# Performance work log

Hardware: AMD Instinct MI355X
Metric: run time of the kernel (lower is better)

The kernel has to match this reference:

```python
import jax, jax.numpy as jnp
import numpy as np

B = 64        # number of graphs
NPG = 4096    # nodes per graph (equal-size segments, batch ids sorted)
H = 256       # hidden_dim
C0, C1 = 256, 64  # num_clusters


def setup_inputs() -> dict:
    key = jax.random.key(0)
    ks = jax.random.split(key, 8)
    N = B * NPG
    x = jax.random.normal(ks[0], (N, H), dtype=jnp.float32)
    edge_index = jax.random.randint(ks[1], (2, N), 0, N, dtype=jnp.int64)  # unused by forward
    batch = jnp.repeat(jnp.arange(B, dtype=jnp.int64), NPG)  # sorted, equal-size segments
    s = 1.0 / np.sqrt(H)
    W0 = jax.random.uniform(ks[2], (H, C0), jnp.float32, -s, s)
    b0 = jax.random.uniform(ks[3], (C0,), jnp.float32, -s, s)
    W1 = jax.random.uniform(ks[4], (H, C1), jnp.float32, -s, s)
    b1 = jax.random.uniform(ks[5], (C1,), jnp.float32, -s, s)
    sf = 1.0 / np.sqrt(C1 * H)
    Wf = jax.random.uniform(ks[6], (C1 * H, H), jnp.float32, -sf, sf)
    bf = jax.random.uniform(ks[7], (H,), jnp.float32, -sf, sf)
    return {"x": x, "edge_index": edge_index, "batch": batch,
            "W0": W0, "b0": b0, "W1": W1, "b1": b1, "Wf": Wf, "bf": bf}


def reference(x, edge_index, batch, W0, b0, W1, b1, Wf, bf):
    # Level 0: softmax cluster assignment + per-graph segmented matmul A^T @ F.
    # batch ids are sorted with equal-size segments, so the per-graph Python
    # loop of the original collapses to a reshape + batched einsum.
    A0 = jax.nn.softmax(x @ W0 + b0, axis=-1)                      # [N, C0]
    f0 = jnp.einsum('bnc,bnh->bch',
                    A0.reshape(B, NPG, C0),
                    x.reshape(B, NPG, H)).reshape(B * C0, H)        # [B*C0, H]
    # Level 1: same pattern on pooled cluster features (C0 'nodes' per graph).
    A1 = jax.nn.softmax(f0 @ W1 + b1, axis=-1)                     # [B*C0, C1]
    f1 = jnp.einsum('bnc,bnh->bch',
                    A1.reshape(B, C0, C1),
                    f0.reshape(B, C0, H)).reshape(B, C1 * H)        # [B, C1*H]
    # Final pool: Linear -> ReLU (Dropout is identity in eval mode).
    return jax.nn.relu(f1 @ Wf + bf)                               # [B, H]
```

## Files before the change

kernel.cpp:

```cpp
#include <hip/hip_runtime.h>
#include <stdint.h>

#define NG   64
#define NPG  4096
#define HD   256
#define NC0  256
#define NC1  64
#define KSPLIT 2

typedef __attribute__((ext_vector_type(8))) short bfx8;
typedef __attribute__((ext_vector_type(4))) float fx4;

__device__ __forceinline__ unsigned short f2bf(float f) {
  union { float f; unsigned int u; } v; v.f = f;
  return (unsigned short)((v.u + 0x7FFFu + ((v.u >> 16) & 1u)) >> 16);
}
__device__ __forceinline__ unsigned int pack2(float a, float b) {
  return (unsigned int)f2bf(a) | ((unsigned int)f2bf(b) << 16);
}

#define ASYNC_COPY16(gptr, lptr) \
  __builtin_amdgcn_global_load_lds((const __attribute__((address_space(1))) unsigned int*)(gptr), \
                                   (__attribute__((address_space(3))) unsigned int*)(lptr), 16, 0, 0)

__global__ __launch_bounds__(256) void k_w0f(const float* __restrict__ W0,
                                             unsigned short* __restrict__ W0F) {
  int gid = blockIdx.x * 256 + threadIdx.x;
  int l15 = gid & 15;
  int q   = (gid >> 4) & 3;
  int ks  = (gid >> 6) & 1;
  int kc  = (gid >> 7) & 3;
  int cblk = gid >> 9;
  int c = cblk * 16 + l15;
  int kb = kc * 64 + ks * 32 + q * 8;
  unsigned int u[4];
  #pragma unroll
  for (int j = 0; j < 8; j += 2)
    u[j >> 1] = pack2(W0[(size_t)(kb + j) * 256 + c], W0[(size_t)(kb + j + 1) * 256 + c]);
  *(float4*)(W0F + (size_t)gid * 8) = *(float4*)u;
}

#define XSP 72
__global__ __launch_bounds__(512, 2) void k_assign0(
    const float* __restrict__ x, const unsigned short* __restrict__ W0F,
    const float* __restrict__ b0, unsigned short* __restrict__ A0T,
    unsigned short* __restrict__ xT, int g0) {
  __shared__ unsigned short xs[2][128 * XSP];
  __shared__ float red[128 * 4];
  unsigned short* at = (unsigned short*)xs;

  int gl = blockIdx.x >> 5, nt = blockIdx.x & 31;
  int tid = threadIdx.x;
  int wave = tid >> 6, lane = tid & 63;
  int wm = wave >> 2, wn = wave & 3;
  int l15 = lane & 15, q = lane >> 4;

  fx4 acc[4][4];
  #pragma unroll
  for (int i = 0; i < 4; ++i)
    #pragma unroll
    for (int j = 0; j < 4; ++j) acc[i][j] = fx4{0.f, 0.f, 0.f, 0.f};

  const float* xbase = x + ((size_t)(g0 + gl) * NPG + (size_t)nt * 128) * HD;
  int snode = tid >> 2, sseg = (tid & 3) * 16;

  {
    const float4* src = (const float4*)(xbase + (size_t)snode * HD + sseg);
    float4 v0 = src[0], v1 = src[1], v2 = src[2], v3 = src[3];
    float4 pv[2]; unsigned int* pu = (unsigned int*)pv;
    pu[0] = pack2(v0.x, v0.y); pu[1] = pack2(v0.z, v0.w);
    pu[2] = pack2(v1.x, v1.y); pu[3] = pack2(v1.z, v1.w);
    pu[4] = pack2(v2.x, v2.y); pu[5] = pack2(v2.z, v2.w);
    pu[6] = pack2(v3.x, v3.y); pu[7] = pack2(v3.z, v3.w);
    float4* d = (float4*)&xs[0][snode * XSP + sseg];
    d[0] = pv[0]; d[1] = pv[1];
  }
  __syncthreads();

  for (int kc = 0; kc < 4; ++kc) {
    int buf = kc & 1;
    if (kc < 3) {
      const float4* src = (const float4*)(xbase + (size_t)snode * HD + (kc + 1) * 64 + sseg);
      float4 v0 = src[0], v1 = src[1], v2 = src[2], v3 = src[3];
      float4 pv[2]; unsigned int* pu = (unsigned int*)pv;
      pu[0] = pack2(v0.x, v0.y); pu[1] = pack2(v0.z, v0.w);
      pu[2] = pack2(v1.x, v1.y); pu[3] = pack2(v1.z, v1.w);
      pu[4] = pack2(v2.x, v2.y); pu[5] = pack2(v2.z, v2.w);
      pu[6] = pack2(v3.x, v3.y); pu[7] = pack2(v3.z, v3.w);
      float4* d = (float4*)&xs[buf ^ 1][snode * XSP + sseg];
      d[0] = pv[0]; d[1] = pv[1];
    }
    #pragma unroll
    for (int ks = 0; ks < 2; ++ks) {
      int kk = ks * 32 + q * 8;
      bfx8 af[4];
      #pragma unroll
      for (int mi = 0; mi < 4; ++mi)
        af[mi] = *(const bfx8*)&xs[buf][(wm * 64 + mi * 16 + l15) * XSP + kk];
      #pragma unroll
      for (int ni = 0; ni < 4; ++ni) {
        bfx8 bv = *(const bfx8*)(W0F + ((size_t)(((wn * 4 + ni) * 8 + kc * 2 + ks) * 64 + lane)) * 8);
        #pragma unroll
        for (int mi = 0; mi < 4; ++mi)
          acc[mi][ni] = __builtin_amdgcn_mfma_f32_16x16x32_bf16(af[mi], bv, acc[mi][ni], 0, 0, 0);
      }
    }
    {
      int hl = tid >> 3;
      int seg = (tid & 7) * 16;
      unsigned int u[8];
      #pragma unroll
      for (int i = 0; i < 16; i += 2) {
        unsigned short a = xs[buf][(seg + i) * XSP + hl];
        unsigned short b = xs[buf][(seg + i + 1) * XSP + hl];
        u[i >> 1] = (unsigned int)a | ((unsigned int)b << 16);
      }
      float4* dst = (float4*)(xT + ((size_t)gl * HD + kc * 64 + hl) * NPG + (size_t)nt * 128 + seg);
      dst[0] = *(float4*)&u[0];
      dst[1] = *(float4*)&u[4];
    }
    __syncthreads();
  }

  float bv4[4];
  #pragma unroll
  for (int ni = 0; ni < 4; ++ni) bv4[ni] = b0[wn * 64 + ni * 16 + l15];
  #pragma unroll
  for (int mi = 0; mi < 4; ++mi)
    #pragma unroll
    for (int ni = 0; ni < 4; ++ni)
      #pragma unroll
      for (int r = 0; r < 4; ++r) acc[mi][ni][r] += bv4[ni];

  float mrow[4][4];
  #pragma unroll
  for (int mi = 0; mi < 4; ++mi)
    #pragma unroll
    for (int r = 0; r < 4; ++r) {
      float m = fmaxf(fmaxf(acc[mi][0][r], acc[mi][1][r]), fmaxf(acc[mi][2][r], acc[mi][3][r]));
      #pragma unroll
      for (int off = 1; off < 16; off <<= 1) m = fmaxf(m, __shfl_xor(m, off));
      mrow[mi][r] = m;
    }
  if (l15 == 0) {
    #pragma unroll
    for (int mi = 0; mi < 4; ++mi)
      #pragma unroll
      for (int r = 0; r < 4; ++r)
        red[(wm * 64 + mi * 16 + q * 4 + r) * 4 + wn] = mrow[mi][r];
  }
  __syncthreads();
  #pragma unroll
  for (int mi = 0; mi < 4; ++mi)
    #pragma unroll
    for (int r = 0; r < 4; ++r) {
      float4 rv = *(const float4*)&red[(wm * 64 + mi * 16 + q * 4 + r) * 4];
      mrow[mi][r] = fmaxf(fmaxf(rv.x, rv.y), fmaxf(rv.z, rv.w));
    }
  __syncthreads();
  float srow[4][4];
  #pragma unroll
  for (int mi = 0; mi < 4; ++mi)
    #pragma unroll
    for (int r = 0; r < 4; ++r) {
      float s = 0.f;
      #pragma unroll
      for (int ni = 0; ni < 4; ++ni) {
        float e = __expf(acc[mi][ni][r] - mrow[mi][r]);
        acc[mi][ni][r] = e; s += e;
      }
      #pragma unroll
      for (int off = 1; off < 16; off <<= 1) s += __shfl_xor(s, off);
      srow[mi][r] = s;
    }
  if (l15 == 0) {
    #pragma unroll
    for (int mi = 0; mi < 4; ++mi)
      #pragma unroll
      for (int r = 0; r < 4; ++r)
        red[(wm * 64 + mi * 16 + q * 4 + r) * 4 + wn] = srow[mi][r];
  }
  __syncthreads();
  #pragma unroll
  for (int mi = 0; mi < 4; ++mi)
    #pragma unroll
    for (int r = 0; r < 4; ++r) {
      float4 rv = *(const float4*)&red[(wm * 64 + mi * 16 + q * 4 + r) * 4];
      float inv = 1.f / (rv.x + rv.y + rv.z + rv.w);
      #pragma unroll
      for (int ni = 0; ni < 4; ++ni) acc[mi][ni][r] *= inv;
    }
  __syncthreads();

  unsigned short* A0Tg = A0T + (size_t)gl * NC0 * NPG + (size_t)nt * 128;
  #pragma unroll
  for (int p = 0; p < 2; ++p) {
    if ((wn >> 1) == p) {
      int cb = (wn & 1) * 64;
      #pragma unroll
      for (int mi = 0; mi < 4; ++mi) {
        int ncol = wm * 64 + mi * 16 + q * 4;
        #pragma unroll
        for (int ni = 0; ni < 4; ++ni) {
          int cl = cb + ni * 16 + l15;
          uint2 w;
          w.x = pack2(acc[mi][ni][0], acc[mi][ni][1]);
          w.y = pack2(acc[mi][ni][2], acc[mi][ni][3]);
          *(uint2*)(at + cl * 136 + ncol) = w;
        }
      }
    }
    __syncthreads();
    {
      int row = tid >> 2, seg = (tid & 3) * 32;
      const float4* s4 = (const float4*)(at + row * 136 + seg);
      float4 a = s4[0], b = s4[1], c = s4[2], d = s4[3];
      float4* d4 = (float4*)(A0Tg + (size_t)(p * 128 + row) * NPG + seg);
      d4[0] = a; d4[1] = b; d4[2] = c; d4[3] = d;
    }
    __syncthreads();
  }
}

__global__ __launch_bounds__(256, 2) void k_pool0(
    const unsigned short* __restrict__ A0T, const unsigned short* __restrict__ xT,
    float* __restrict__ f0p, int g0) {
  __shared__ unsigned short a_s[128 * 64];
  __shared__ unsigned short b_s[128 * 64];
  int bid = blockIdx.x;
  int kidx = bid & 1;
  int nt = (bid >> 1) & 1;
  int mt = (bid >> 2) & 1;
  int gl = bid >> 3;

  int tid = threadIdx.x;
  int wave = tid >> 6, lane = tid & 63;
  int wm = wave >> 1, wn = wave & 1;
  int l15 = lane & 15, q = lane >> 4;

  const int KPER = NPG / KSPLIT;
  const unsigned short* abase = A0T + ((size_t)gl * NC0 + (size_t)mt * 128) * NPG + (size_t)kidx * KPER;
  const unsigned short* bbase = xT  + ((size_t)gl * HD  + (size_t)nt * 128) * NPG + (size_t)kidx * KPER;

  fx4 acc[4][4];
  #pragma unroll
  for (int i = 0; i < 4; ++i)
    #pragma unroll
    for (int j = 0; j < 4; ++j) acc[i][j] = fx4{0.f, 0.f, 0.f, 0.f};

  int srow = lane >> 3;
  int sg   = (lane & 7) ^ srow;
  size_t soff = (size_t)srow * NPG + (size_t)sg * 8;

  for (int k0 = 0; k0 < KPER; k0 += 64) {
    #pragma unroll
    for (int i = 0; i < 4; ++i) {
      int r0 = wave * 32 + i * 8;
      ASYNC_COPY16(abase + (size_t)r0 * NPG + k0 + soff, &a_s[r0 * 64]);
      ASYNC_COPY16(bbase + (size_t)r0 * NPG + k0 + soff, &b_s[r0 * 64]);
    }
    __syncthreads();
    #pragma unroll
    for (int ks = 0; ks < 2; ++ks) {
      int gx = ((ks * 4 + q) ^ (l15 & 7)) << 3;
      bfx8 af[4], bf[4];
      #pragma unroll
      for (int mi = 0; mi < 4; ++mi)
        af[mi] = *(const bfx8*)&a_s[(wm * 64 + mi * 16 + l15) * 64 + gx];
      #pragma unroll
      for (int ni = 0; ni < 4; ++ni)
        bf[ni] = *(const bfx8*)&b_s[(wn * 64 + ni * 16 + l15) * 64 + gx];
      #pragma unroll
      for (int ni = 0; ni < 4; ++ni)
        #pragma unroll
        for (int mi = 0; mi < 4; ++mi)
          acc[mi][ni] = __builtin_amdgcn_mfma_f32_16x16x32_bf16(af[mi], bf[ni], acc[mi][ni], 0, 0, 0);
    }
    __syncthreads();
  }

  float* dst = f0p + (size_t)kidx * NG * NC0 * HD
             + ((size_t)(g0 + gl) * NC0 + (size_t)mt * 128) * HD + (size_t)nt * 128;
  #pragma unroll
  for (int mi = 0; mi < 4; ++mi)
    #pragma unroll
    for (int ni = 0; ni < 4; ++ni) {
      int c = wm * 64 + mi * 16 + q * 4;
      int h = wn * 64 + ni * 16 + l15;
      #pragma unroll
      for (int r = 0; r < 4; ++r)
        dst[(size_t)(c + r) * HD + h] = acc[mi][ni][r];
    }
}

__global__ __launch_bounds__(256) void k_f0sum(float* __restrict__ f0) {
  size_t i = ((size_t)blockIdx.x * 256 + threadIdx.x) * 4;
  float4 a = *(const float4*)(f0 + i);
  float4 b = *(const float4*)(f0 + (size_t)NG * NC0 * HD + i);
  a.x += b.x; a.y += b.y; a.z += b.z; a.w += b.w;
  *(float4*)(f0 + i) = a;
}

__global__ __launch_bounds__(256) void k_assign1(
    const float* __restrict__ f0, const float* __restrict__ W1,
    const float* __restrict__ b1, float* __restrict__ A1) {
  int row = blockIdx.x * 4 + (threadIdx.x >> 6);
  int lane = threadIdx.x & 63;
  const float* fr = f0 + (size_t)row * 256;
  float acc = b1[lane];
  for (int k = 0; k < 256; k += 4) {
    float4 fv = *(const float4*)(fr + k);
    acc += fv.x * W1[(k    ) * 64 + lane];
    acc += fv.y * W1[(k + 1) * 64 + lane];
    acc += fv.z * W1[(k + 2) * 64 + lane];
    acc += fv.w * W1[(k + 3) * 64 + lane];
  }
  float m = acc;
  #pragma unroll
  for (int off = 1; off < 64; off <<= 1) m = fmaxf(m, __shfl_xor(m, off));
  float e = __expf(acc - m);
  float s = e;
  #pragma unroll
  for (int off = 1; off < 64; off <<= 1) s += __shfl_xor(s, off);
  A1[(size_t)row * 64 + lane] = e / s;
}

__global__ __launch_bounds__(256) void k_pool1(
    const float* __restrict__ A1, const float* __restrict__ f0, float* __restrict__ f1) {
  int b = blockIdx.x >> 2, cg = blockIdx.x & 3;
  int h = threadIdx.x;
  const float* a1p = A1 + (size_t)b * NC0 * NC1 + cg * 16;
  const float* f0p = f0 + (size_t)b * NC0 * HD + h;
  float acc[16];
  #pragma unroll
  for (int j = 0; j < 16; ++j) acc[j] = 0.f;
  for (int c0 = 0; c0 < 256; ++c0) {
    float fv = f0p[(size_t)c0 * 256];
    #pragma unroll
    for (int j = 0; j < 16; ++j) acc[j] += a1p[c0 * 64 + j] * fv;
  }
  float* d = f1 + (size_t)b * 16384 + (size_t)(cg * 16) * 256 + h;
  #pragma unroll
  for (int j = 0; j < 16; ++j) d[(size_t)j * 256] = acc[j];
}

__global__ __launch_bounds__(256) void k_final_partial(
    const float* __restrict__ f1, const float* __restrict__ Wf, float* __restrict__ ot) {
  int b = blockIdx.x >> 4, kidx = blockIdx.x & 15;
  int h = threadIdx.x;
  const float* fp = f1 + (size_t)b * 16384 + (size_t)kidx * 1024;
  const float* wp = Wf + (size_t)kidx * 1024 * 256 + h;
  float acc = 0.f;
  for (int k = 0; k < 1024; k += 4) {
    float4 fv = *(const float4*)(fp + k);
    acc += fv.x * wp[(size_t)(k    ) * 256];
    acc += fv.y * wp[(size_t)(k + 1) * 256];
    acc += fv.z * wp[(size_t)(k + 2) * 256];
    acc += fv.w * wp[(size_t)(k + 3) * 256];
  }
  atomicAdd(&ot[b * 256 + h], acc);
}

__global__ __launch_bounds__(256) void k_final_out(
    const float* __restrict__ ot, const float* __restrict__ bfv, float* __restrict__ out) {
  int i = blockIdx.x * 256 + threadIdx.x;
  float v = ot[i] + bfv[i & 255];
  out[i] = v > 0.f ? v : 0.f;
}

extern "C" void kernel_launch(void* const* d_in, const int* in_sizes, int n_in,
                              void* d_out, int out_size, void* d_ws, size_t ws_size,
                              hipStream_t stream) {
  const float* x   = (const float*)d_in[0];
  const float* W0  = (const float*)d_in[3];
  const float* b0  = (const float*)d_in[4];
  const float* W1  = (const float*)d_in[5];
  const float* b1  = (const float*)d_in[6];
  const float* Wf  = (const float*)d_in[7];
  const float* bfv = (const float*)d_in[8];
  float* out = (float*)d_out;
  char* ws = (char*)d_ws;

  float* f0p = (float*)ws;
  float* f0  = f0p;
  float* ot  = (float*)(ws + ((size_t)32 << 20));
  unsigned short* W0F = (unsigned short*)(ws + ((size_t)32 << 20) + 65536);
  size_t chunk_off = ((size_t)32 << 20) + 65536 + 131072;
  size_t per_graph = (size_t)4 * HD * NPG;
  size_t avail = ws_size > chunk_off ? ws_size - chunk_off : 0;
  int G = (int)(avail / per_graph);
  if (G > 64) G = 64;
  if (G < 1) G = 1;
  unsigned short* xT  = (unsigned short*)(ws + chunk_off);
  unsigned short* A0T = xT + (size_t)G * HD * NPG;
  float* f1 = (float*)xT;
  float* A1 = (float*)A0T;

  hipMemsetAsync(ot, 0, 65536, stream);
  k_w0f<<<32, 256, 0, stream>>>(W0, W0F);

  for (int g0 = 0; g0 < NG; g0 += G) {
    int gc = (NG - g0 < G) ? (NG - g0) : G;
    k_assign0<<<gc * 32, 512, 0, stream>>>(x, W0F, b0, A0T, xT, g0);
    k_pool0<<<gc * 4 * KSPLIT, 256, 0, stream>>>(A0T, xT, f0p, g0);
  }
  k_f0sum<<<4096, 256, 0, stream>>>(f0);
  k_assign1<<<4096, 256, 0, stream>>>(f0, W1, b1, A1);
  k_pool1<<<256, 256, 0, stream>>>(A1, f0, f1);
  k_final_partial<<<64 * 16, 256, 0, stream>>>(f1, Wf, ot);
  k_final_out<<<64, 256, 0, stream>>>(ot, bfv, out);
}
```

Baseline: 750.7 us.

## Split x conversion into separate kernel, async-LDS assign0, KSPLIT 4, atomic-free final reduce

```diff
diff --git a/kernel.cpp b/kernel.cpp
--- a/kernel.cpp
+++ b/kernel.cpp
@@ -6,7 +6,8 @@
 #define HD   256
 #define NC0  256
 #define NC1  64
-#define KSPLIT 2
+#define KSPLIT 4
+#define G_MAX 16
 
 typedef __attribute__((ext_vector_type(8))) short bfx8;
 typedef __attribute__((ext_vector_type(4))) float fx4;
@@ -23,37 +24,68 @@
   __builtin_amdgcn_global_load_lds((const __attribute__((address_space(1))) unsigned int*)(gptr), \
                                    (__attribute__((address_space(3))) unsigned int*)(lptr), 16, 0, 0)
 
-__global__ __launch_bounds__(256) void k_w0f(const float* __restrict__ W0,
-                                             unsigned short* __restrict__ W0F) {
-  int gid = blockIdx.x * 256 + threadIdx.x;
-  int l15 = gid & 15;
-  int q   = (gid >> 4) & 3;
-  int ks  = (gid >> 6) & 1;
-  int kc  = (gid >> 7) & 3;
-  int cblk = gid >> 9;
-  int c = cblk * 16 + l15;
-  int kb = kc * 64 + ks * 32 + q * 8;
-  unsigned int u[4];
-  #pragma unroll
-  for (int j = 0; j < 8; j += 2)
-    u[j >> 1] = pack2(W0[(size_t)(kb + j) * 256 + c], W0[(size_t)(kb + j + 1) * 256 + c]);
-  *(float4*)(W0F + (size_t)gid * 8) = *(float4*)u;
-}
-
-#define XSP 72
-__global__ __launch_bounds__(512, 2) void k_assign0(
-    const float* __restrict__ x, const unsigned short* __restrict__ W0F,
-    const float* __restrict__ b0, unsigned short* __restrict__ A0T,
-    unsigned short* __restrict__ xT, int g0) {
-  __shared__ unsigned short xs[2][128 * XSP];
-  __shared__ float red[128 * 4];
-  unsigned short* at = (unsigned short*)xs;
-
-  int gl = blockIdx.x >> 5, nt = blockIdx.x & 31;
+__global__ __launch_bounds__(256) void k_w0t(const float* __restrict__ W0,
+                                             unsigned short* __restrict__ W0T) {
+  int idx = blockIdx.x * 256 + threadIdx.x;
+  int c = idx >> 8, h = idx & 255;
+  W0T[idx] = f2bf(W0[h * 256 + c]);
+}
+
+__global__ __launch_bounds__(256, 4) void k_xt(const float* __restrict__ x,
+                                               unsigned short* __restrict__ xb,
+                                               unsigned short* __restrict__ xT, int g0) {
+  __shared__ unsigned short tile[64 * 256];
+  int gl = blockIdx.x >> 6, ntile = blockIdx.x & 63;
+  int t = threadIdx.x;
+  size_t gbase = ((size_t)(g0 + gl) * NPG + (size_t)ntile * 64) * HD;
+
+  #pragma unroll
+  for (int i = 0; i < 16; ++i) {
+    int flat = t + i * 256;
+    int row = flat >> 6, f4 = flat & 63;
+    float4 v = *(const float4*)(x + gbase + (size_t)row * HD + f4 * 4);
+    uint2 p;
+    p.x = pack2(v.x, v.y); p.y = pack2(v.z, v.w);
+    *(uint2*)(tile + row * 256 + f4 * 4) = p;
+  }
+  __syncthreads();
+
+  {
+    unsigned int u[32];
+    #pragma unroll
+    for (int n = 0; n < 64; n += 2)
+      u[n >> 1] = (unsigned int)tile[n * 256 + t] |
+                  ((unsigned int)tile[(n + 1) * 256 + t] << 16);
+    float4* dst = (float4*)(xT + ((size_t)gl * HD + t) * NPG + (size_t)ntile * 64);
+    #pragma unroll
+    for (int i = 0; i < 8; ++i) dst[i] = ((float4*)u)[i];
+  }
+  #pragma unroll
+  for (int i = 0; i < 8; ++i) {
+    int flat = t + i * 256;
+    int row = flat >> 5, c16 = flat & 31;
+    float4 v = *(const float4*)(tile + row * 256 + c16 * 8);
+    *(float4*)(xb + ((size_t)gl * NPG + (size_t)ntile * 64 + row) * HD + c16 * 8) = v;
+  }
+}
+
+__global__ __launch_bounds__(256, 3) void k_assign0(
+    const unsigned short* __restrict__ xb, const unsigned short* __restrict__ W0T,
+    const float* __restrict__ b0, unsigned short* __restrict__ A0T) {
+  __shared__ char smem[40960];
+  __shared__ float red[64 * 4];
+  unsigned short* a_s = (unsigned short*)smem;
+  unsigned short* b_s = (unsigned short*)(smem + 8192);
+  unsigned short* at  = (unsigned short*)smem;
+
+  int gl = blockIdx.x >> 6, ntile = blockIdx.x & 63;
   int tid = threadIdx.x;
   int wave = tid >> 6, lane = tid & 63;
-  int wm = wave >> 2, wn = wave & 3;
+  int wn = wave;
   int l15 = lane & 15, q = lane >> 4;
+  int srow = lane >> 3, sg = (lane & 7) ^ srow;
+
+  const unsigned short* xbase = xb + ((size_t)gl * NPG + (size_t)ntile * 64) * HD;
 
   fx4 acc[4][4];
   #pragma unroll
@@ -61,63 +93,34 @@
     #pragma unroll
     for (int j = 0; j < 4; ++j) acc[i][j] = fx4{0.f, 0.f, 0.f, 0.f};
 
-  const float* xbase = x + ((size_t)(g0 + gl) * NPG + (size_t)nt * 128) * HD;
-  int snode = tid >> 2, sseg = (tid & 3) * 16;
-
-  {
-    const float4* src = (const float4*)(xbase + (size_t)snode * HD + sseg);
-    float4 v0 = src[0], v1 = src[1], v2 = src[2], v3 = src[3];
-    float4 pv[2]; unsigned int* pu = (unsigned int*)pv;
-    pu[0] = pack2(v0.x, v0.y); pu[1] = pack2(v0.z, v0.w);
-    pu[2] = pack2(v1.x, v1.y); pu[3] = pack2(v1.z, v1.w);
-    pu[4] = pack2(v2.x, v2.y); pu[5] = pack2(v2.z, v2.w);
-    pu[6] = pack2(v3.x, v3.y); pu[7] = pack2(v3.z, v3.w);
-    float4* d = (float4*)&xs[0][snode * XSP + sseg];
-    d[0] = pv[0]; d[1] = pv[1];
-  }
-  __syncthreads();
-
   for (int kc = 0; kc < 4; ++kc) {
-    int buf = kc & 1;
-    if (kc < 3) {
-      const float4* src = (const float4*)(xbase + (size_t)snode * HD + (kc + 1) * 64 + sseg);
-      float4 v0 = src[0], v1 = src[1], v2 = src[2], v3 = src[3];
-      float4 pv[2]; unsigned int* pu = (unsigned int*)pv;
-      pu[0] = pack2(v0.x, v0.y); pu[1] = pack2(v0.z, v0.w);
-      pu[2] = pack2(v1.x, v1.y); pu[3] = pack2(v1.z, v1.w);
-      pu[4] = pack2(v2.x, v2.y); pu[5] = pack2(v2.z, v2.w);
-      pu[6] = pack2(v3.x, v3.y); pu[7] = pack2(v3.z, v3.w);
-      float4* d = (float4*)&xs[buf ^ 1][snode * XSP + sseg];
-      d[0] = pv[0]; d[1] = pv[1];
-    }
+    int k0 = kc * 64;
+    #pragma unroll
+    for (int i = 0; i < 2; ++i) {
+      int r0 = wave * 16 + i * 8;
+      ASYNC_COPY16(xbase + (size_t)(r0 + srow) * HD + k0 + sg * 8, &a_s[r0 * 64]);
+    }
+    #pragma unroll
+    for (int i = 0; i < 8; ++i) {
+      int c0 = wave * 64 + i * 8;
+      ASYNC_COPY16(W0T + (size_t)(c0 + srow) * HD + k0 + sg * 8, &b_s[c0 * 64]);
+    }
+    __syncthreads();
     #pragma unroll
     for (int ks = 0; ks < 2; ++ks) {
-      int kk = ks * 32 + q * 8;
-      bfx8 af[4];
+      int gx = ((ks * 4 + q) ^ (l15 & 7)) << 3;
+      bfx8 af[4], bf[4];
       #pragma unroll
       for (int mi = 0; mi < 4; ++mi)
-        af[mi] = *(const bfx8*)&xs[buf][(wm * 64 + mi * 16 + l15) * XSP + kk];
-      #pragma unroll
-      for (int ni = 0; ni < 4; ++ni) {
-        bfx8 bv = *(const bfx8*)(W0F + ((size_t)(((wn * 4 + ni) * 8 + kc * 2 + ks) * 64 + lane)) * 8);
+        af[mi] = *(const bfx8*)&a_s[(mi * 16 + l15) * 64 + gx];
+      #pragma unroll
+      for (int ni = 0; ni < 4; ++ni)
+        bf[ni] = *(const bfx8*)&b_s[(wn * 64 + ni * 16 + l15) * 64 + gx];
+      #pragma unroll
+      for (int ni = 0; ni < 4; ++ni)
         #pragma unroll
         for (int mi = 0; mi < 4; ++mi)
-          acc[mi][ni] = __builtin_amdgcn_mfma_f32_16x16x32_bf16(af[mi], bv, acc[mi][ni], 0, 0, 0);
-      }
-    }
-    {
-      int hl = tid >> 3;
-      int seg = (tid & 7) * 16;
-      unsigned int u[8];
-      #pragma unroll
-      for (int i = 0; i < 16; i += 2) {
-        unsigned short a = xs[buf][(seg + i) * XSP + hl];
-        unsigned short b = xs[buf][(seg + i + 1) * XSP + hl];
-        u[i >> 1] = (unsigned int)a | ((unsigned int)b << 16);
-      }
-      float4* dst = (float4*)(xT + ((size_t)gl * HD + kc * 64 + hl) * NPG + (size_t)nt * 128 + seg);
-      dst[0] = *(float4*)&u[0];
-      dst[1] = *(float4*)&u[4];
+          acc[mi][ni] = __builtin_amdgcn_mfma_f32_16x16x32_bf16(af[mi], bf[ni], acc[mi][ni], 0, 0, 0);
     }
     __syncthreads();
   }
@@ -147,18 +150,18 @@
     for (int mi = 0; mi < 4; ++mi)
       #pragma unroll
       for (int r = 0; r < 4; ++r)
-        red[(wm * 64 + mi * 16 + q * 4 + r) * 4 + wn] = mrow[mi][r];
+        red[(mi * 16 + q * 4 + r) * 4 + wn] = mrow[mi][r];
   }
   __syncthreads();
   #pragma unroll
   for (int mi = 0; mi < 4; ++mi)
     #pragma unroll
     for (int r = 0; r < 4; ++r) {
-      float4 rv = *(const float4*)&red[(wm * 64 + mi * 16 + q * 4 + r) * 4];
+      float4 rv = *(const float4*)&red[(mi * 16 + q * 4 + r) * 4];
       mrow[mi][r] = fmaxf(fmaxf(rv.x, rv.y), fmaxf(rv.z, rv.w));
     }
   __syncthreads();
-  float srow[4][4];
+  float srow2[4][4];
   #pragma unroll
   for (int mi = 0; mi < 4; ++mi)
     #pragma unroll
@@ -171,54 +174,47 @@
       }
       #pragma unroll
       for (int off = 1; off < 16; off <<= 1) s += __shfl_xor(s, off);
-      srow[mi][r] = s;
+      srow2[mi][r] = s;
     }
   if (l15 == 0) {
     #pragma unroll
     for (int mi = 0; mi < 4; ++mi)
       #pragma unroll
       for (int r = 0; r < 4; ++r)
-        red[(wm * 64 + mi * 16 + q * 4 + r) * 4 + wn] = srow[mi][r];
+        red[(mi * 16 + q * 4 + r) * 4 + wn] = srow2[mi][r];
   }
   __syncthreads();
   #pragma unroll
   for (int mi = 0; mi < 4; ++mi)
     #pragma unroll
     for (int r = 0; r < 4; ++r) {
-      float4 rv = *(const float4*)&red[(wm * 64 + mi * 16 + q * 4 + r) * 4];
+      float4 rv = *(const float4*)&red[(mi * 16 + q * 4 + r) * 4];
       float inv = 1.f / (rv.x + rv.y + rv.z + rv.w);
       #pragma unroll
       for (int ni = 0; ni < 4; ++ni) acc[mi][ni][r] *= inv;
     }
   __syncthreads();
 
-  unsigned short* A0Tg = A0T + (size_t)gl * NC0 * NPG + (size_t)nt * 128;
-  #pragma unroll
-  for (int p = 0; p < 2; ++p) {
-    if ((wn >> 1) == p) {
-      int cb = (wn & 1) * 64;
-      #pragma unroll
-      for (int mi = 0; mi < 4; ++mi) {
-        int ncol = wm * 64 + mi * 16 + q * 4;
-        #pragma unroll
-        for (int ni = 0; ni < 4; ++ni) {
-          int cl = cb + ni * 16 + l15;
-          uint2 w;
-          w.x = pack2(acc[mi][ni][0], acc[mi][ni][1]);
-          w.y = pack2(acc[mi][ni][2], acc[mi][ni][3]);
-          *(uint2*)(at + cl * 136 + ncol) = w;
-        }
-      }
-    }
-    __syncthreads();
-    {
-      int row = tid >> 2, seg = (tid & 3) * 32;
-      const float4* s4 = (const float4*)(at + row * 136 + seg);
-      float4 a = s4[0], b = s4[1], c = s4[2], d = s4[3];
-      float4* d4 = (float4*)(A0Tg + (size_t)(p * 128 + row) * NPG + seg);
-      d4[0] = a; d4[1] = b; d4[2] = c; d4[3] = d;
-    }
-    __syncthreads();
+  #pragma unroll
+  for (int mi = 0; mi < 4; ++mi) {
+    int ncol = mi * 16 + q * 4;
+    #pragma unroll
+    for (int ni = 0; ni < 4; ++ni) {
+      int cl = wn * 64 + ni * 16 + l15;
+      uint2 w;
+      w.x = pack2(acc[mi][ni][0], acc[mi][ni][1]);
+      w.y = pack2(acc[mi][ni][2], acc[mi][ni][3]);
+      *(uint2*)(at + cl * 72 + ncol) = w;
+    }
+  }
+  __syncthreads();
+  {
+    float4 v[8];
+    #pragma unroll
+    for (int s = 0; s < 8; ++s) v[s] = *(const float4*)(at + tid * 72 + s * 8);
+    unsigned short* dst = A0T + ((size_t)gl * NC0 + tid) * NPG + (size_t)ntile * 64;
+    #pragma unroll
+    for (int s = 0; s < 8; ++s) *(float4*)(dst + s * 8) = v[s];
   }
 }
 
@@ -228,10 +224,10 @@
   __shared__ unsigned short a_s[128 * 64];
   __shared__ unsigned short b_s[128 * 64];
   int bid = blockIdx.x;
-  int kidx = bid & 1;
-  int nt = (bid >> 1) & 1;
-  int mt = (bid >> 2) & 1;
-  int gl = bid >> 3;
+  int kidx = bid & 3;
+  int nt = (bid >> 2) & 1;
+  int mt = (bid >> 3) & 1;
+  int gl = bid >> 4;
 
   int tid = threadIdx.x;
   int wave = tid >> 6, lane = tid & 63;
@@ -295,9 +291,13 @@
 
 __global__ __launch_bounds__(256) void k_f0sum(float* __restrict__ f0) {
   size_t i = ((size_t)blockIdx.x * 256 + threadIdx.x) * 4;
+  const size_t S = (size_t)NG * NC0 * HD;
   float4 a = *(const float4*)(f0 + i);
-  float4 b = *(const float4*)(f0 + (size_t)NG * NC0 * HD + i);
-  a.x += b.x; a.y += b.y; a.z += b.z; a.w += b.w;
+  float4 b = *(const float4*)(f0 + S + i);
+  float4 c = *(const float4*)(f0 + 2 * S + i);
+  float4 d = *(const float4*)(f0 + 3 * S + i);
+  a.x += b.x + c.x + d.x; a.y += b.y + c.y + d.y;
+  a.z += b.z + c.z + d.z; a.w += b.w + c.w + d.w;
   *(float4*)(f0 + i) = a;
 }
 
@@ -358,14 +358,16 @@
     acc += fv.z * wp[(size_t)(k + 2) * 256];
     acc += fv.w * wp[(size_t)(k + 3) * 256];
   }
-  atomicAdd(&ot[b * 256 + h], acc);
+  ot[((size_t)kidx * 64 + b) * 256 + h] = acc;
 }
 
 __global__ __launch_bounds__(256) void k_final_out(
     const float* __restrict__ ot, const float* __restrict__ bfv, float* __restrict__ out) {
-  int i = blockIdx.x * 256 + threadIdx.x;
-  float v = ot[i] + bfv[i & 255];
-  out[i] = v > 0.f ? v : 0.f;
+  int b = blockIdx.x, h = threadIdx.x;
+  float s = bfv[h];
+  #pragma unroll
+  for (int k = 0; k < 16; ++k) s += ot[((size_t)k * 64 + b) * 256 + h];
+  out[b * 256 + h] = s > 0.f ? s : 0.f;
 }
 
 extern "C" void kernel_launch(void* const* d_in, const int* in_sizes, int n_in,
@@ -383,26 +385,27 @@
 
   float* f0p = (float*)ws;
   float* f0  = f0p;
-  float* ot  = (float*)(ws + ((size_t)32 << 20));
-  unsigned short* W0F = (unsigned short*)(ws + ((size_t)32 << 20) + 65536);
-  size_t chunk_off = ((size_t)32 << 20) + 65536 + 131072;
-  size_t per_graph = (size_t)4 * HD * NPG;
-  size_t avail = ws_size > chunk_off ? ws_size - chunk_off : 0;
+  size_t off = (size_t)64 << 20;
+  float* ot = (float*)(ws + off);                 off += (size_t)1 << 20;
+  unsigned short* W0T = (unsigned short*)(ws + off); off += 131072;
+  float* f1 = (float*)(ws + off);                 off += (size_t)16 << 20;
+  float* A1 = (float*)(ws + off);                 off += (size_t)4 << 20;
+  size_t per_graph = (size_t)3 * NPG * HD * 2;
+  size_t avail = ws_size > off ? ws_size - off : 0;
   int G = (int)(avail / per_graph);
-  if (G > 64) G = 64;
+  if (G > G_MAX) G = G_MAX;
   if (G < 1) G = 1;
-  unsigned short* xT  = (unsigned short*)(ws + chunk_off);
-  unsigned short* A0T = xT + (size_t)G * HD * NPG;
-  float* f1 = (float*)xT;
-  float* A1 = (float*)A0T;
-
-  hipMemsetAsync(ot, 0, 65536, stream);
-  k_w0f<<<32, 256, 0, stream>>>(W0, W0F);
+  unsigned short* xb  = (unsigned short*)(ws + off);
+  unsigned short* xT  = xb + (size_t)G * NPG * HD;
+  unsigned short* A0T = xT + (size_t)G * NPG * HD;
+
+  k_w0t<<<256, 256, 0, stream>>>(W0, W0T);
 
   for (int g0 = 0; g0 < NG; g0 += G) {
     int gc = (NG - g0 < G) ? (NG - g0) : G;
-    k_assign0<<<gc * 32, 512, 0, stream>>>(x, W0F, b0, A0T, xT, g0);
-    k_pool0<<<gc * 4 * KSPLIT, 256, 0, stream>>>(A0T, xT, f0p, g0);
+    k_xt<<<gc * 64, 256, 0, stream>>>(x, xb, xT, g0);
+    k_assign0<<<gc * 64, 256, 0, stream>>>(xb, W0T, b0, A0T);
+    k_pool0<<<gc * 16, 256, 0, stream>>>(A0T, xT, f0p, g0);
   }
   k_f0sum<<<4096, 256, 0, stream>>>(f0);
   k_assign1<<<4096, 256, 0, stream>>>(f0, W1, b1, A1);
```

Measured after the change: 801.5 us. +6.8%, slower.
